# Optimization experiments

Hardware: AMD Instinct MI355X
Metric: run time of the kernel (lower is better)

The kernel has to match this reference:

```python
import jax, jax.numpy as jnp
import numpy as np

N = 50000      # nodes
R = 3          # relation types
E = 200000     # edges per relation
DIN, DHID, DOUT = 128, 128, 64


def _hetero_graphconv(x, src, dst, W, b):
    """Sum over relations of dgl GraphConv(norm='both') applied per relation.
    x:[N,d_in], src/dst:[R,E], W:[R,d_in,d_out], b:[R,d_out] -> [N,d_out]"""
    Rr, Ee = src.shape
    n = x.shape[0]
    off = (jnp.arange(Rr) * n)[:, None]            # per-relation segment offset
    src_f = (src + off).reshape(-1)                # [R*E]
    dst_f = (dst + off).reshape(-1)
    ones = jnp.ones((Rr * Ee,), x.dtype)
    out_deg = jax.ops.segment_sum(ones, src_f, num_segments=Rr * n).reshape(Rr, n)
    in_deg = jax.ops.segment_sum(ones, dst_f, num_segments=Rr * n).reshape(Rr, n)
    out_norm = jnp.maximum(out_deg, 1.0) ** -0.5   # dgl clamps deg to min 1
    in_norm = jnp.maximum(in_deg, 1.0) ** -0.5
    # gather src features, scaled by per-relation out-degree norm: [R,E,d_in]
    msgs = x[src] * jnp.take_along_axis(out_norm, src, axis=1)[..., None]
    agg = jax.ops.segment_sum(msgs.reshape(Rr * Ee, -1), dst_f,
                              num_segments=Rr * n).reshape(Rr, n, -1)
    agg = agg * in_norm[..., None]                 # [R,N,d_in]
    # per-relation linear then sum over relations (HeteroGraphConv 'sum')
    return jnp.einsum('rnd,rdo->no', agg, W) + b.sum(axis=0)


def setup_inputs() -> dict:
    key = jax.random.key(0)
    ks = jax.random.split(key, 7)
    x = jax.random.normal(ks[0], (N, DIN), jnp.float32)
    src = jax.random.randint(ks[1], (R, E), 0, N)
    dst = jax.random.randint(ks[2], (R, E), 0, N)
    W1 = jax.random.normal(ks[3], (R, DIN, DHID), jnp.float32) / np.sqrt(DIN).astype(np.float32)
    b1 = jax.random.normal(ks[4], (R, DHID), jnp.float32) * 0.01
    W2 = jax.random.normal(ks[5], (R, DHID, DOUT), jnp.float32) / np.sqrt(DHID).astype(np.float32)
    b2 = jax.random.normal(ks[6], (R, DOUT), jnp.float32) * 0.01
    return {"x": x, "W1": W1, "b1": b1, "W2": W2, "b2": b2, "src": src, "dst": dst}


def reference(x, W1, b1, W2, b2, src, dst):
    h = jax.nn.relu(_hetero_graphconv(x, src, dst, W1, b1))
    return _hetero_graphconv(h, src, dst, W2, b2)
```

## Files before the change

### kernel.cpp

```cpp
#include <hip/hip_runtime.h>

#define N_NODES 50000
#define N_REL   3
#define N_EDGE  200000
#define RN      (N_REL * N_NODES)
#define RE      (N_REL * N_EDGE)
#define GEMM1_BLKS 782
#define DEG_BLKS   2344
#define SCAN_BLOCKS 49
#define FUSE_CHUNKS 98
#define PREP_BLKS  288

typedef short bf16x8 __attribute__((ext_vector_type(8)));
typedef float f32x4  __attribute__((ext_vector_type(4)));

__device__ __forceinline__ unsigned short f2bf(float f) {
    unsigned u = __float_as_uint(f);
    u = (u + 0x7fffu + ((u >> 16) & 1u)) >> 16;
    return (unsigned short)u;
}
__device__ __forceinline__ unsigned pack_bf2(float lo, float hi) {
    return (unsigned)f2bf(lo) | ((unsigned)f2bf(hi) << 16);
}

__device__ __forceinline__ void wtrans_one(
    const float* __restrict__ W, unsigned short* __restrict__ Wtf, int ncols, int i)
{
    int rel = i / (128 * ncols);
    int rem = i - rel * 128 * ncols;
    int k   = rem / ncols;
    int n   = rem - k * ncols;
    int f   = (rel * (ncols / 16) + (n >> 4)) * 4 + (k >> 5);
    int idx = f * 512 + ((k & 31) >> 3) * 128 + (n & 15) * 8 + (k & 7);
    Wtf[idx] = f2bf(W[i]);
}

__global__ __launch_bounds__(256) void prep_kernel(
    const float* __restrict__ W1, unsigned short* __restrict__ Wt1,
    const float* __restrict__ W2, unsigned short* __restrict__ Wt2,
    float* __restrict__ zbuf, int* __restrict__ done)
{
    int i = blockIdx.x * 256 + threadIdx.x;
    if (i == 0) *done = 0;
    for (int q = i; q < 2 * RN; q += PREP_BLKS * 256) zbuf[q] = 0.f;
    if (i < 3 * 128 * 128) {
        wtrans_one(W1, Wt1, 128, i);
    } else {
        int j = i - 3 * 128 * 128;
        if (j < 3 * 128 * 64) wtrans_one(W2, Wt2, 64, j);
    }
}

template <bool ABF16, int NCOLS>
__device__ __forceinline__ void gemm_body(
    const void* __restrict__ Av, const unsigned short* __restrict__ Wtf,
    unsigned short* __restrict__ Y, int nrows, int mt,
    unsigned* As, unsigned* Ws0, unsigned* Ws1)
{
    const int tid = threadIdx.x;
    const uint4* Wt4 = (const uint4*)Wtf;

    if constexpr (ABF16) {
        const uint4* Ab = (const uint4*)Av;
        #pragma unroll
        for (int p = 0; p < 4; ++p) {
            int q   = p * 256 + tid;
            int row = q >> 4, w4 = q & 15;
            int gr  = mt + row;
            uint4 v = make_uint4(0u, 0u, 0u, 0u);
            if (gr < nrows) v = Ab[(size_t)gr * 16 + w4];
            As[row * 68 + w4 * 4 + 0] = v.x;
            As[row * 68 + w4 * 4 + 1] = v.y;
            As[row * 68 + w4 * 4 + 2] = v.z;
            As[row * 68 + w4 * 4 + 3] = v.w;
        }
    } else {
        const float* A = (const float*)Av;
        #pragma unroll
        for (int p = 0; p < 16; ++p) {
            int q   = tid + p * 256;
            int row = q >> 6, wc = q & 63;
            int gr  = mt + row;
            float2 v = make_float2(0.f, 0.f);
            if (gr < nrows) v = *reinterpret_cast<const float2*>(&A[(size_t)gr * 128 + wc * 2]);
            As[row * 68 + wc] = pack_bf2(v.x, v.y);
        }
    }

    #pragma unroll
    for (int p = 0; p < 4; ++p) {
        uint4 v = Wt4[tid + p * 256];
        *reinterpret_cast<uint4*>(&Ws0[(tid + p * 256) * 4]) = v;
    }
    __syncthreads();

    const int w  = tid >> 6;
    const int l  = tid & 63;
    const int g  = l >> 4;
    const int lr = l & 15;
    const int ar = w * 16 + lr;

    bf16x8 a[4];
    #pragma unroll
    for (int kb = 0; kb < 4; ++kb)
        a[kb] = *reinterpret_cast<const bf16x8*>(&As[ar * 68 + kb * 16 + g * 4]);

    constexpr int TPR  = NCOLS / 16;
    constexpr int NGRP = 3 * NCOLS / 64;
    const int boff = (g * 16 + lr) * 4;

    unsigned* wc_buf = Ws0;
    unsigned* wn_buf = Ws1;
    #pragma unroll 1
    for (int grp = 0; grp < NGRP; ++grp) {
        uint4 st[4];
        if (grp + 1 < NGRP) {
            #pragma unroll
            for (int p = 0; p < 4; ++p)
                st[p] = Wt4[(grp + 1) * 1024 + tid + p * 256];
        }

        f32x4 acc[4];
        #pragma unroll
        for (int ct4 = 0; ct4 < 4; ++ct4) {
            acc[ct4] = (f32x4){0.f, 0.f, 0.f, 0.f};
            #pragma unroll
            for (int kb = 0; kb < 4; ++kb) {
                bf16x8 b = *reinterpret_cast<const bf16x8*>(
                    &wc_buf[(ct4 * 4 + kb) * 256 + boff]);
                acc[ct4] = __builtin_amdgcn_mfma_f32_16x16x32_bf16(a[kb], b, acc[ct4], 0, 0, 0);
            }
        }

        int gct0 = grp * 4;
        int rel  = gct0 / TPR;
        int cb   = (gct0 % TPR) * 16;
        #pragma unroll
        for (int i = 0; i < 4; ++i) {
            int grow = mt + w * 16 + g * 4 + i;
            if (grow < nrows) {
                size_t rowbase = ((size_t)rel * N_NODES + grow) * NCOLS + cb;
                #pragma unroll
                for (int ct4 = 0; ct4 < 4; ++ct4)
                    Y[rowbase + ct4 * 16 + lr] = f2bf(acc[ct4][i]);
            }
        }

        if (grp + 1 < NGRP) {
            #pragma unroll
            for (int p = 0; p < 4; ++p)
                *reinterpret_cast<uint4*>(&wn_buf[(tid + p * 256) * 4]) = st[p];
        }
        __syncthreads();
        unsigned* t = wc_buf; wc_buf = wn_buf; wn_buf = t;
    }
}

template <bool ABF16, int NCOLS>
__global__ __launch_bounds__(256) void gemm_mfma(
    const void* __restrict__ Av, const unsigned short* __restrict__ Wtf,
    unsigned short* __restrict__ Y, int nrows)
{
    __shared__ unsigned As[64 * 68];
    __shared__ unsigned Ws[2][4096];
    gemm_body<ABF16, NCOLS>(Av, Wtf, Y, nrows, blockIdx.x * 64, As, Ws[0], Ws[1]);
}

__device__ __forceinline__ void gemm1_body_light(
    const float* __restrict__ A, const unsigned short* __restrict__ Wtf,
    unsigned short* __restrict__ Y, int mt, unsigned* Ws)
{
    const int tid = threadIdx.x;
    const uint4* Wt4 = (const uint4*)Wtf;
    const int w  = tid >> 6;
    const int l  = tid & 63;
    const int g  = l >> 4;
    const int lr = l & 15;
    const int arow = mt + w * 16 + lr;
    const bool rowok = arow < N_NODES;

    bf16x8 a[4];
    #pragma unroll
    for (int kb = 0; kb < 4; ++kb) {
        float4 v0 = make_float4(0.f, 0.f, 0.f, 0.f);
        float4 v1 = make_float4(0.f, 0.f, 0.f, 0.f);
        if (rowok) {
            const float* ap = &A[(size_t)arow * 128 + kb * 32 + g * 8];
            v0 = *reinterpret_cast<const float4*>(ap);
            v1 = *reinterpret_cast<const float4*>(ap + 4);
        }
        union { unsigned u[4]; bf16x8 v; } cv;
        cv.u[0] = pack_bf2(v0.x, v0.y);
        cv.u[1] = pack_bf2(v0.z, v0.w);
        cv.u[2] = pack_bf2(v1.x, v1.y);
        cv.u[3] = pack_bf2(v1.z, v1.w);
        a[kb] = cv.v;
    }

    const int boff = (g * 16 + lr) * 4;

    #pragma unroll 1
    for (int grp = 0; grp < 6; ++grp) {
        __syncthreads();
        #pragma unroll
        for (int p = 0; p < 4; ++p) {
            uint4 v = Wt4[grp * 1024 + tid + p * 256];
            *reinterpret_cast<uint4*>(&Ws[(tid + p * 256) * 4]) = v;
        }
        __syncthreads();

        f32x4 acc[4];
        #pragma unroll
        for (int ct4 = 0; ct4 < 4; ++ct4) {
            acc[ct4] = (f32x4){0.f, 0.f, 0.f, 0.f};
            #pragma unroll
            for (int kb = 0; kb < 4; ++kb) {
                bf16x8 b = *reinterpret_cast<const bf16x8*>(
                    &Ws[(ct4 * 4 + kb) * 256 + boff]);
                acc[ct4] = __builtin_amdgcn_mfma_f32_16x16x32_bf16(a[kb], b, acc[ct4], 0, 0, 0);
            }
        }

        int rel = grp >> 1;
        int cb  = (grp & 1) * 64;
        #pragma unroll
        for (int i = 0; i < 4; ++i) {
            int grow = mt + w * 16 + g * 4 + i;
            if (grow < N_NODES) {
                size_t rowbase = ((size_t)rel * N_NODES + grow) * 128 + cb;
                #pragma unroll
                for (int ct4 = 0; ct4 < 4; ++ct4)
                    Y[rowbase + ct4 * 16 + lr] = f2bf(acc[ct4][i]);
            }
        }
    }
}

__global__ __launch_bounds__(256) void fused_gemm1_deg(
    const float* __restrict__ x, const unsigned short* __restrict__ Wt1,
    unsigned short* __restrict__ Y,
    const int* __restrict__ src, const int* __restrict__ dst,
    float* __restrict__ odeg, float* __restrict__ ideg,
    unsigned short* __restrict__ rank)
{
    __shared__ unsigned Ws[4096];

    const int c = blockIdx.x >> 5;
    const int o = blockIdx.x & 31;

    if (o < 8) {
        int gb = c * 8 + o;
        if (gb >= GEMM1_BLKS) return;
        gemm1_body_light(x, Wt1, Y, gb * 64, Ws);
    } else {
        int db = c * 24 + (o - 8);
        int i  = db * 256 + threadIdx.x;
        if (i < RE) {
            int r = i / N_EDGE;
            int s = src[i], t = dst[i];
            unsafeAtomicAdd(&odeg[r * N_NODES + s], 1.0f);
            float old = unsafeAtomicAdd(&ideg[r * N_NODES + t], 1.0f);
            rank[i] = (unsigned short)(int)old;
        }
    }
}

__global__ __launch_bounds__(256) void scan_all_kernel(
    float* __restrict__ odeg, float* __restrict__ ideg,
    int* __restrict__ off, int* __restrict__ roff,
    int* __restrict__ bsums, int* __restrict__ done)
{
    __shared__ int tsum[256];
    __shared__ int addsh;
    const int tid  = threadIdx.x;
    const int base = blockIdx.x * 1024 + tid * 4;

    float c0[4], c1[4], c2[4];
    int tot[4], s = 0;
    #pragma unroll
    for (int j = 0; j < 4; ++j) {
        int idx = base + j;
        if (idx < N_NODES) {
            c0[j] = ideg[idx];
            c1[j] = ideg[N_NODES + idx];
            c2[j] = ideg[2 * N_NODES + idx];
            tot[j] = (int)c0[j] + (int)c1[j] + (int)c2[j];
        } else { c0[j] = c1[j] = c2[j] = 0.f; tot[j] = 0; }
        s += tot[j];
    }
    tsum[tid] = s;
    __syncthreads();
    #pragma unroll
    for (int d = 1; d < 256; d <<= 1) {
        int v   = tsum[tid];
        int add = (tid >= d) ? tsum[tid - d] : 0;
        __syncthreads();
        tsum[tid] = v + add;
        __syncthreads();
    }
    int run = tsum[tid] - s;

    if (tid == 255) bsums[blockIdx.x] = tsum[255];
    __threadfence();
    if (tid == 0) {
        __hip_atomic_fetch_add(done, 1, __ATOMIC_RELEASE, __HIP_MEMORY_SCOPE_AGENT);
        while (__hip_atomic_load(done, __ATOMIC_ACQUIRE, __HIP_MEMORY_SCOPE_AGENT) < SCAN_BLOCKS)
            __builtin_amdgcn_s_sleep(2);
    }
    __syncthreads();

    if (tid < 64) {
        int v = (tid < blockIdx.x) ? bsums[tid] : 0;
        #pragma unroll
        for (int d = 32; d > 0; d >>= 1) v += __shfl_down(v, d, 64);
        if (tid == 0) addsh = v;
    }
    __syncthreads();
    int run2 = run + addsh;

    #pragma unroll
    for (int j = 0; j < 4; ++j) {
        int t = base + j;
        if (t < N_NODES) {
            off[t]                = run2;
            roff[t]               = run2;
            roff[N_NODES + t]     = run2 + (int)c0[j];
            roff[2 * N_NODES + t] = run2 + (int)c0[j] + (int)c1[j];
            ideg[t]               = rsqrtf(fmaxf(c0[j], 1.0f));
            ideg[N_NODES + t]     = rsqrtf(fmaxf(c1[j], 1.0f));
            ideg[2 * N_NODES + t] = rsqrtf(fmaxf(c2[j], 1.0f));
            run2 += tot[j];
        }
    }
    if (blockIdx.x == 0 && tid == 0) off[N_NODES] = RE;

    int q0 = blockIdx.x * 256 + tid;
    for (int q = q0; q < RN; q += SCAN_BLOCKS * 256)
        odeg[q] = rsqrtf(fmaxf(odeg[q], 1.0f));
}

__global__ __launch_bounds__(256) void fill_kernel(
    const int* __restrict__ src, const int* __restrict__ dst,
    const float* __restrict__ onorm, const float* __restrict__ inorm,
    const int* __restrict__ roff, const unsigned short* __restrict__ rank,
    unsigned* __restrict__ csr)
{
    int i = blockIdx.x * 256 + threadIdx.x;
    if (i >= N_EDGE) return;
    int r   = blockIdx.y;
    int idx = r * N_EDGE + i;
    int s = src[idx], t = dst[idx];
    float wv = onorm[r * N_NODES + s] * inorm[r * N_NODES + t];
    int slot = roff[r * N_NODES + t] + (int)rank[idx];
    csr[slot] = ((unsigned)s << 16) | (unsigned)f2bf(wv);
}

__global__ __launch_bounds__(256) void agg128_kernel(
    const unsigned* __restrict__ Y, const unsigned* __restrict__ csr,
    const int* __restrict__ off, const int* __restrict__ roff,
    const float* __restrict__ b, unsigned* __restrict__ hbf)
{
    int wid  = (blockIdx.x * 256 + threadIdx.x) >> 6;
    int lane = threadIdx.x & 63;
    if (wid >= N_NODES) return;

    int e   = off[wid], end = off[wid + 1];
    int r1  = roff[N_NODES + wid];
    int r2  = roff[2 * N_NODES + wid];
    float a0 = 0.f, a1 = 0.f;

    for (; e + 8 <= end; e += 8) {
        unsigned p[8]; unsigned y[8];
        #pragma unroll
        for (int j = 0; j < 8; ++j) p[j] = csr[e + j];
        #pragma unroll
        for (int j = 0; j < 8; ++j) {
            int rr = (e + j >= r1) + (e + j >= r2);
            y[j] = Y[((size_t)rr * N_NODES + (p[j] >> 16)) * 64 + lane];
        }
        #pragma unroll
        for (int j = 0; j < 8; ++j) {
            float wv = __uint_as_float((p[j] & 0xffffu) << 16);
            a0 = fmaf(wv, __uint_as_float(y[j] << 16), a0);
            a1 = fmaf(wv, __uint_as_float(y[j] & 0xffff0000u), a1);
        }
    }
    if (e + 4 <= end) {
        unsigned p[4]; unsigned y[4];
        #pragma unroll
        for (int j = 0; j < 4; ++j) p[j] = csr[e + j];
        #pragma unroll
        for (int j = 0; j < 4; ++j) {
            int rr = (e + j >= r1) + (e + j >= r2);
            y[j] = Y[((size_t)rr * N_NODES + (p[j] >> 16)) * 64 + lane];
        }
        #pragma unroll
        for (int j = 0; j < 4; ++j) {
            float wv = __uint_as_float((p[j] & 0xffffu) << 16);
            a0 = fmaf(wv, __uint_as_float(y[j] << 16), a0);
            a1 = fmaf(wv, __uint_as_float(y[j] & 0xffff0000u), a1);
        }
        e += 4;
    }
    for (; e < end; ++e) {
        unsigned p = csr[e];
        int rr = (e >= r1) + (e >= r2);
        unsigned y = Y[((size_t)rr * N_NODES + (p >> 16)) * 64 + lane];
        float wv = __uint_as_float((p & 0xffffu) << 16);
        a0 = fmaf(wv, __uint_as_float(y << 16), a0);
        a1 = fmaf(wv, __uint_as_float(y & 0xffff0000u), a1);
    }

    int d = lane * 2;
    float o0 = a0 + b[d]     + b[128 + d]     + b[256 + d];
    float o1 = a1 + b[d + 1] + b[128 + d + 1] + b[256 + d + 1];
    hbf[(size_t)wid * 64 + lane] = pack_bf2(fmaxf(o0, 0.f), fmaxf(o1, 0.f));
}

__global__ __launch_bounds__(256) void agg64_kernel(
    const unsigned short* __restrict__ Y, const unsigned* __restrict__ csr,
    const int* __restrict__ off, const int* __restrict__ roff,
    const float* __restrict__ b, float* __restrict__ out)
{
    int wid  = (blockIdx.x * 256 + threadIdx.x) >> 6;
    int lane = threadIdx.x & 63;
    if (wid >= N_NODES) return;

    int e   = off[wid], end = off[wid + 1];
    int r1  = roff[N_NODES + wid];
    int r2  = roff[2 * N_NODES + wid];
    float a = 0.f;

    for (; e + 8 <= end; e += 8) {
        unsigned p[8]; unsigned short y[8];
        #pragma unroll
        for (int j = 0; j < 8; ++j) p[j] = csr[e + j];
        #pragma unroll
        for (int j = 0; j < 8; ++j) {
            int rr = (e + j >= r1) + (e + j >= r2);
            y[j] = Y[((size_t)rr * N_NODES + (p[j] >> 16)) * 64 + lane];
        }
        #pragma unroll
        for (int j = 0; j < 8; ++j)
            a = fmaf(__uint_as_float((p[j] & 0xffffu) << 16),
                     __uint_as_float(((unsigned)y[j]) << 16), a);
    }
    if (e + 4 <= end) {
        unsigned p[4]; unsigned short y[4];
        #pragma unroll
        for (int j = 0; j < 4; ++j) p[j] = csr[e + j];
        #pragma unroll
        for (int j = 0; j < 4; ++j) {
            int rr = (e + j >= r1) + (e + j >= r2);
            y[j] = Y[((size_t)rr * N_NODES + (p[j] >> 16)) * 64 + lane];
        }
        #pragma unroll
        for (int j = 0; j < 4; ++j)
            a = fmaf(__uint_as_float((p[j] & 0xffffu) << 16),
                     __uint_as_float(((unsigned)y[j]) << 16), a);
        e += 4;
    }
    for (; e < end; ++e) {
        unsigned p = csr[e];
        int rr = (e >= r1) + (e >= r2);
        a = fmaf(__uint_as_float((p & 0xffffu) << 16),
                 __uint_as_float(((unsigned)Y[((size_t)rr * N_NODES + (p >> 16)) * 64 + lane]) << 16), a);
    }

    float bs = b[lane] + b[64 + lane] + b[128 + lane];
    out[(size_t)wid * 64 + lane] = a + bs;
}

extern "C" void kernel_launch(void* const* d_in, const int* in_sizes, int n_in,
                              void* d_out, int out_size, void* d_ws, size_t ws_size,
                              hipStream_t stream)
{
    const float* x   = (const float*)d_in[0];
    const float* W1  = (const float*)d_in[1];
    const float* b1  = (const float*)d_in[2];
    const float* W2  = (const float*)d_in[3];
    const float* b2  = (const float*)d_in[4];
    const int*   src = (const int*)d_in[5];
    const int*   dst = (const int*)d_in[6];
    float*       out = (float*)d_out;

    char* w = (char*)d_ws;
    float* onorm  = (float*)w;                 w += (size_t)RN * 4;
    float* inorm  = (float*)w;                 w += (size_t)RN * 4;
    int*   off    = (int*)w;                   w += (size_t)(N_NODES + 1) * 4;
    int*   roff   = (int*)w;                   w += (size_t)RN * 4;
    int*   bsums  = (int*)w;                   w += 512;
    int*   done   = (int*)w;                   w += 512;
    unsigned short* rank = (unsigned short*)w; w += (size_t)RE * 2;
    w = (char*)(((uintptr_t)w + 255) & ~(uintptr_t)255);
    unsigned* csr = (unsigned*)w;              w += (size_t)RE * 4;
    unsigned* hbf = (unsigned*)w;              w += (size_t)N_NODES * 64 * 4;
    unsigned short* Ybf = (unsigned short*)w;  w += (size_t)N_REL * N_NODES * 128 * 2;
    unsigned short* Wt1 = (unsigned short*)w;  w += (size_t)N_REL * 128 * 128 * 2;
    unsigned short* Wt2 = (unsigned short*)w;

    prep_kernel<<<PREP_BLKS, 256, 0, stream>>>(W1, Wt1, W2, Wt2, onorm, done);

    fused_gemm1_deg<<<FUSE_CHUNKS * 32, 256, 0, stream>>>(
        x, Wt1, Ybf, src, dst, onorm, inorm, rank);

    scan_all_kernel<<<SCAN_BLOCKS, 256, 0, stream>>>(onorm, inorm, off, roff, bsums, done);

    fill_kernel<<<dim3((N_EDGE + 255) / 256, N_REL), 256, 0, stream>>>(
        src, dst, onorm, inorm, roff, rank, csr);

    agg128_kernel<<<(N_NODES + 3) / 4, 256, 0, stream>>>(
        (const unsigned*)Ybf, csr, off, roff, b1, hbf);

    gemm_mfma<true, 64><<<GEMM1_BLKS, 256, 0, stream>>>(hbf, Wt2, Ybf, N_NODES);
    agg64_kernel<<<(N_NODES + 3) / 4, 256, 0, stream>>>(Ybf, csr, off, roff, b2, out);
}
```

Measured before the change: 261.2 us.

## Fuse scan with CSR fill and fuse layer-1 aggregation with layer-2 GEMM

Result: slower. 342.3 us (+31.1%).

```diff
diff --git a/kernel.cpp b/kernel.cpp
--- a/kernel.cpp
+++ b/kernel.cpp
@@ -6,9 +6,8 @@
 #define RN      (N_REL * N_NODES)
 #define RE      (N_REL * N_EDGE)
 #define GEMM1_BLKS 782
-#define DEG_BLKS   2344
-#define SCAN_BLOCKS 49
 #define FUSE_CHUNKS 98
+#define SF_BLOCKS 196
 #define PREP_BLKS  288
 
 typedef short bf16x8 __attribute__((ext_vector_type(8)));
@@ -41,7 +40,7 @@
     float* __restrict__ zbuf, int* __restrict__ done)
 {
     int i = blockIdx.x * 256 + threadIdx.x;
-    if (i == 0) *done = 0;
+    if (i < 2) done[i] = 0;
     for (int q = i; q < 2 * RN; q += PREP_BLKS * 256) zbuf[q] = 0.f;
     if (i < 3 * 128 * 128) {
         wtrans_one(W1, Wt1, 128, i);
@@ -49,121 +48,6 @@
         int j = i - 3 * 128 * 128;
         if (j < 3 * 128 * 64) wtrans_one(W2, Wt2, 64, j);
     }
-}
-
-template <bool ABF16, int NCOLS>
-__device__ __forceinline__ void gemm_body(
-    const void* __restrict__ Av, const unsigned short* __restrict__ Wtf,
-    unsigned short* __restrict__ Y, int nrows, int mt,
-    unsigned* As, unsigned* Ws0, unsigned* Ws1)
-{
-    const int tid = threadIdx.x;
-    const uint4* Wt4 = (const uint4*)Wtf;
-
-    if constexpr (ABF16) {
-        const uint4* Ab = (const uint4*)Av;
-        #pragma unroll
-        for (int p = 0; p < 4; ++p) {
-            int q   = p * 256 + tid;
-            int row = q >> 4, w4 = q & 15;
-            int gr  = mt + row;
-            uint4 v = make_uint4(0u, 0u, 0u, 0u);
-            if (gr < nrows) v = Ab[(size_t)gr * 16 + w4];
-            As[row * 68 + w4 * 4 + 0] = v.x;
-            As[row * 68 + w4 * 4 + 1] = v.y;
-            As[row * 68 + w4 * 4 + 2] = v.z;
-            As[row * 68 + w4 * 4 + 3] = v.w;
-        }
-    } else {
-        const float* A = (const float*)Av;
-        #pragma unroll
-        for (int p = 0; p < 16; ++p) {
-            int q   = tid + p * 256;
-            int row = q >> 6, wc = q & 63;
-            int gr  = mt + row;
-            float2 v = make_float2(0.f, 0.f);
-            if (gr < nrows) v = *reinterpret_cast<const float2*>(&A[(size_t)gr * 128 + wc * 2]);
-            As[row * 68 + wc] = pack_bf2(v.x, v.y);
-        }
-    }
-
-    #pragma unroll
-    for (int p = 0; p < 4; ++p) {
-        uint4 v = Wt4[tid + p * 256];
-        *reinterpret_cast<uint4*>(&Ws0[(tid + p * 256) * 4]) = v;
-    }
-    __syncthreads();
-
-    const int w  = tid >> 6;
-    const int l  = tid & 63;
-    const int g  = l >> 4;
-    const int lr = l & 15;
-    const int ar = w * 16 + lr;
-
-    bf16x8 a[4];
-    #pragma unroll
-    for (int kb = 0; kb < 4; ++kb)
-        a[kb] = *reinterpret_cast<const bf16x8*>(&As[ar * 68 + kb * 16 + g * 4]);
-
-    constexpr int TPR  = NCOLS / 16;
-    constexpr int NGRP = 3 * NCOLS / 64;
-    const int boff = (g * 16 + lr) * 4;
-
-    unsigned* wc_buf = Ws0;
-    unsigned* wn_buf = Ws1;
-    #pragma unroll 1
-    for (int grp = 0; grp < NGRP; ++grp) {
-        uint4 st[4];
-        if (grp + 1 < NGRP) {
-            #pragma unroll
-            for (int p = 0; p < 4; ++p)
-                st[p] = Wt4[(grp + 1) * 1024 + tid + p * 256];
-        }
-
-        f32x4 acc[4];
-        #pragma unroll
-        for (int ct4 = 0; ct4 < 4; ++ct4) {
-            acc[ct4] = (f32x4){0.f, 0.f, 0.f, 0.f};
-            #pragma unroll
-            for (int kb = 0; kb < 4; ++kb) {
-                bf16x8 b = *reinterpret_cast<const bf16x8*>(
-                    &wc_buf[(ct4 * 4 + kb) * 256 + boff]);
-                acc[ct4] = __builtin_amdgcn_mfma_f32_16x16x32_bf16(a[kb], b, acc[ct4], 0, 0, 0);
-            }
-        }
-
-        int gct0 = grp * 4;
-        int rel  = gct0 / TPR;
-        int cb   = (gct0 % TPR) * 16;
-        #pragma unroll
-        for (int i = 0; i < 4; ++i) {
-            int grow = mt + w * 16 + g * 4 + i;
-            if (grow < nrows) {
-                size_t rowbase = ((size_t)rel * N_NODES + grow) * NCOLS + cb;
-                #pragma unroll
-                for (int ct4 = 0; ct4 < 4; ++ct4)
-                    Y[rowbase + ct4 * 16 + lr] = f2bf(acc[ct4][i]);
-            }
-        }
-
-        if (grp + 1 < NGRP) {
-            #pragma unroll
-            for (int p = 0; p < 4; ++p)
-                *reinterpret_cast<uint4*>(&wn_buf[(tid + p * 256) * 4]) = st[p];
-        }
-        __syncthreads();
-        unsigned* t = wc_buf; wc_buf = wn_buf; wn_buf = t;
-    }
-}
-
-template <bool ABF16, int NCOLS>
-__global__ __launch_bounds__(256) void gemm_mfma(
-    const void* __restrict__ Av, const unsigned short* __restrict__ Wtf,
-    unsigned short* __restrict__ Y, int nrows)
-{
-    __shared__ unsigned As[64 * 68];
-    __shared__ unsigned Ws[2][4096];
-    gemm_body<ABF16, NCOLS>(Av, Wtf, Y, nrows, blockIdx.x * 64, As, Ws[0], Ws[1]);
 }
 
 __device__ __forceinline__ void gemm1_body_light(
@@ -265,30 +149,28 @@
     }
 }
 
-__global__ __launch_bounds__(256) void scan_all_kernel(
+__global__ __launch_bounds__(256) void scan_fill_kernel(
     float* __restrict__ odeg, float* __restrict__ ideg,
     int* __restrict__ off, int* __restrict__ roff,
-    int* __restrict__ bsums, int* __restrict__ done)
+    int* __restrict__ bsums, int* __restrict__ done,
+    const int* __restrict__ src, const int* __restrict__ dst,
+    const unsigned short* __restrict__ rank, unsigned* __restrict__ csr)
 {
     __shared__ int tsum[256];
     __shared__ int addsh;
     const int tid  = threadIdx.x;
-    const int base = blockIdx.x * 1024 + tid * 4;
-
-    float c0[4], c1[4], c2[4];
-    int tot[4], s = 0;
-    #pragma unroll
-    for (int j = 0; j < 4; ++j) {
-        int idx = base + j;
-        if (idx < N_NODES) {
-            c0[j] = ideg[idx];
-            c1[j] = ideg[N_NODES + idx];
-            c2[j] = ideg[2 * N_NODES + idx];
-            tot[j] = (int)c0[j] + (int)c1[j] + (int)c2[j];
-        } else { c0[j] = c1[j] = c2[j] = 0.f; tot[j] = 0; }
-        s += tot[j];
-    }
-    tsum[tid] = s;
+    const int bid  = blockIdx.x;
+    const int node = bid * 256 + tid;
+
+    float c0 = 0.f, c1 = 0.f, c2 = 0.f;
+    int tot = 0;
+    if (node < N_NODES) {
+        c0 = ideg[node];
+        c1 = ideg[N_NODES + node];
+        c2 = ideg[2 * N_NODES + node];
+        tot = (int)c0 + (int)c1 + (int)c2;
+    }
+    tsum[tid] = tot;
     __syncthreads();
     #pragma unroll
     for (int d = 1; d < 256; d <<= 1) {
@@ -298,123 +180,201 @@
         tsum[tid] = v + add;
         __syncthreads();
     }
-    int run = tsum[tid] - s;
-
-    if (tid == 255) bsums[blockIdx.x] = tsum[255];
+    const int lexcl = tsum[tid] - tot;
+    if (tid == 255) bsums[bid] = tsum[255];
+
+    if (node < N_NODES) {
+        ideg[node]               = rsqrtf(fmaxf(c0, 1.0f));
+        ideg[N_NODES + node]     = rsqrtf(fmaxf(c1, 1.0f));
+        ideg[2 * N_NODES + node] = rsqrtf(fmaxf(c2, 1.0f));
+    }
+    for (int q = bid * 256 + tid; q < RN; q += SF_BLOCKS * 256)
+        odeg[q] = rsqrtf(fmaxf(odeg[q], 1.0f));
+
+    __syncthreads();
     __threadfence();
     if (tid == 0) {
-        __hip_atomic_fetch_add(done, 1, __ATOMIC_RELEASE, __HIP_MEMORY_SCOPE_AGENT);
-        while (__hip_atomic_load(done, __ATOMIC_ACQUIRE, __HIP_MEMORY_SCOPE_AGENT) < SCAN_BLOCKS)
+        __hip_atomic_fetch_add(&done[0], 1, __ATOMIC_RELEASE, __HIP_MEMORY_SCOPE_AGENT);
+        while (__hip_atomic_load(&done[0], __ATOMIC_ACQUIRE, __HIP_MEMORY_SCOPE_AGENT) < SF_BLOCKS)
             __builtin_amdgcn_s_sleep(2);
     }
     __syncthreads();
 
-    if (tid < 64) {
-        int v = (tid < blockIdx.x) ? bsums[tid] : 0;
-        #pragma unroll
-        for (int d = 32; d > 0; d >>= 1) v += __shfl_down(v, d, 64);
-        if (tid == 0) addsh = v;
-    }
-    __syncthreads();
-    int run2 = run + addsh;
-
+    int bv = (tid < SF_BLOCKS) ? bsums[tid] : 0;
+    tsum[tid] = bv;
+    __syncthreads();
     #pragma unroll
-    for (int j = 0; j < 4; ++j) {
-        int t = base + j;
-        if (t < N_NODES) {
-            off[t]                = run2;
-            roff[t]               = run2;
-            roff[N_NODES + t]     = run2 + (int)c0[j];
-            roff[2 * N_NODES + t] = run2 + (int)c0[j] + (int)c1[j];
-            ideg[t]               = rsqrtf(fmaxf(c0[j], 1.0f));
-            ideg[N_NODES + t]     = rsqrtf(fmaxf(c1[j], 1.0f));
-            ideg[2 * N_NODES + t] = rsqrtf(fmaxf(c2[j], 1.0f));
-            run2 += tot[j];
-        }
-    }
-    if (blockIdx.x == 0 && tid == 0) off[N_NODES] = RE;
-
-    int q0 = blockIdx.x * 256 + tid;
-    for (int q = q0; q < RN; q += SCAN_BLOCKS * 256)
-        odeg[q] = rsqrtf(fmaxf(odeg[q], 1.0f));
-}
-
-__global__ __launch_bounds__(256) void fill_kernel(
-    const int* __restrict__ src, const int* __restrict__ dst,
-    const float* __restrict__ onorm, const float* __restrict__ inorm,
-    const int* __restrict__ roff, const unsigned short* __restrict__ rank,
-    unsigned* __restrict__ csr)
-{
-    int i = blockIdx.x * 256 + threadIdx.x;
-    if (i >= N_EDGE) return;
-    int r   = blockIdx.y;
-    int idx = r * N_EDGE + i;
-    int s = src[idx], t = dst[idx];
-    float wv = onorm[r * N_NODES + s] * inorm[r * N_NODES + t];
-    int slot = roff[r * N_NODES + t] + (int)rank[idx];
-    csr[slot] = ((unsigned)s << 16) | (unsigned)f2bf(wv);
-}
-
-__global__ __launch_bounds__(256) void agg128_kernel(
-    const unsigned* __restrict__ Y, const unsigned* __restrict__ csr,
+    for (int d = 1; d < 256; d <<= 1) {
+        int v   = tsum[tid];
+        int add = (tid >= d) ? tsum[tid - d] : 0;
+        __syncthreads();
+        tsum[tid] = v + add;
+        __syncthreads();
+    }
+    if (tid == 0) addsh = (bid == 0) ? 0 : tsum[bid - 1];
+    __syncthreads();
+
+    const int gbase = lexcl + addsh;
+    if (node < N_NODES) {
+        off[node]                = gbase;
+        roff[node]               = gbase;
+        roff[N_NODES + node]     = gbase + (int)c0;
+        roff[2 * N_NODES + node] = gbase + (int)c0 + (int)c1;
+    }
+    if (bid == 0 && tid == 0) off[N_NODES] = RE;
+
+    __syncthreads();
+    __threadfence();
+    if (tid == 0) {
+        __hip_atomic_fetch_add(&done[1], 1, __ATOMIC_RELEASE, __HIP_MEMORY_SCOPE_AGENT);
+        while (__hip_atomic_load(&done[1], __ATOMIC_ACQUIRE, __HIP_MEMORY_SCOPE_AGENT) < SF_BLOCKS)
+            __builtin_amdgcn_s_sleep(2);
+    }
+    __syncthreads();
+
+    for (int q = bid * 256 + tid; q < RE; q += SF_BLOCKS * 256) {
+        int r = q / N_EDGE;
+        int s = src[q], t = dst[q];
+        float wv = odeg[r * N_NODES + s] * ideg[r * N_NODES + t];
+        int slot = roff[r * N_NODES + t] + (int)rank[q];
+        csr[slot] = ((unsigned)s << 16) | (unsigned)f2bf(wv);
+    }
+}
+
+__global__ __launch_bounds__(256) void layer2_fused(
+    const unsigned* __restrict__ Y1, const unsigned* __restrict__ csr,
     const int* __restrict__ off, const int* __restrict__ roff,
-    const float* __restrict__ b, unsigned* __restrict__ hbf)
-{
-    int wid  = (blockIdx.x * 256 + threadIdx.x) >> 6;
-    int lane = threadIdx.x & 63;
-    if (wid >= N_NODES) return;
-
-    int e   = off[wid], end = off[wid + 1];
-    int r1  = roff[N_NODES + wid];
-    int r2  = roff[2 * N_NODES + wid];
-    float a0 = 0.f, a1 = 0.f;
-
-    for (; e + 8 <= end; e += 8) {
-        unsigned p[8]; unsigned y[8];
-        #pragma unroll
-        for (int j = 0; j < 8; ++j) p[j] = csr[e + j];
-        #pragma unroll
-        for (int j = 0; j < 8; ++j) {
-            int rr = (e + j >= r1) + (e + j >= r2);
-            y[j] = Y[((size_t)rr * N_NODES + (p[j] >> 16)) * 64 + lane];
-        }
-        #pragma unroll
-        for (int j = 0; j < 8; ++j) {
-            float wv = __uint_as_float((p[j] & 0xffffu) << 16);
-            a0 = fmaf(wv, __uint_as_float(y[j] << 16), a0);
-            a1 = fmaf(wv, __uint_as_float(y[j] & 0xffff0000u), a1);
-        }
-    }
-    if (e + 4 <= end) {
-        unsigned p[4]; unsigned y[4];
-        #pragma unroll
-        for (int j = 0; j < 4; ++j) p[j] = csr[e + j];
-        #pragma unroll
-        for (int j = 0; j < 4; ++j) {
-            int rr = (e + j >= r1) + (e + j >= r2);
-            y[j] = Y[((size_t)rr * N_NODES + (p[j] >> 16)) * 64 + lane];
-        }
-        #pragma unroll
-        for (int j = 0; j < 4; ++j) {
-            float wv = __uint_as_float((p[j] & 0xffffu) << 16);
-            a0 = fmaf(wv, __uint_as_float(y[j] << 16), a0);
-            a1 = fmaf(wv, __uint_as_float(y[j] & 0xffff0000u), a1);
-        }
-        e += 4;
-    }
-    for (; e < end; ++e) {
-        unsigned p = csr[e];
-        int rr = (e >= r1) + (e >= r2);
-        unsigned y = Y[((size_t)rr * N_NODES + (p >> 16)) * 64 + lane];
-        float wv = __uint_as_float((p & 0xffffu) << 16);
-        a0 = fmaf(wv, __uint_as_float(y << 16), a0);
-        a1 = fmaf(wv, __uint_as_float(y & 0xffff0000u), a1);
-    }
-
-    int d = lane * 2;
-    float o0 = a0 + b[d]     + b[128 + d]     + b[256 + d];
-    float o1 = a1 + b[d + 1] + b[128 + d + 1] + b[256 + d + 1];
-    hbf[(size_t)wid * 64 + lane] = pack_bf2(fmaxf(o0, 0.f), fmaxf(o1, 0.f));
+    const float* __restrict__ b, const unsigned short* __restrict__ Wt2,
+    unsigned short* __restrict__ Y2)
+{
+    __shared__ unsigned As[64 * 68];
+    __shared__ unsigned Ws[2][4096];
+
+    const int tid = threadIdx.x;
+    const int mt  = blockIdx.x * 64;
+    const uint4* Wt4 = (const uint4*)Wt2;
+
+    #pragma unroll
+    for (int p = 0; p < 4; ++p) {
+        uint4 v = Wt4[tid + p * 256];
+        *reinterpret_cast<uint4*>(&Ws[0][(tid + p * 256) * 4]) = v;
+    }
+
+    const int w    = tid >> 6;
+    const int lane = tid & 63;
+
+    #pragma unroll 1
+    for (int i = 0; i < 16; ++i) {
+        int node = mt + w * 16 + i;
+        unsigned packed = 0u;
+        if (node < N_NODES) {
+            int e  = off[node], end = off[node + 1];
+            int r1 = roff[N_NODES + node];
+            int r2 = roff[2 * N_NODES + node];
+            float a0 = 0.f, a1 = 0.f;
+
+            for (; e + 8 <= end; e += 8) {
+                unsigned p[8]; unsigned y[8];
+                #pragma unroll
+                for (int j = 0; j < 8; ++j) p[j] = csr[e + j];
+                #pragma unroll
+                for (int j = 0; j < 8; ++j) {
+                    int rr = (e + j >= r1) + (e + j >= r2);
+                    y[j] = Y1[((size_t)rr * N_NODES + (p[j] >> 16)) * 64 + lane];
+                }
+                #pragma unroll
+                for (int j = 0; j < 8; ++j) {
+                    float wv = __uint_as_float((p[j] & 0xffffu) << 16);
+                    a0 = fmaf(wv, __uint_as_float(y[j] << 16), a0);
+                    a1 = fmaf(wv, __uint_as_float(y[j] & 0xffff0000u), a1);
+                }
+            }
+            if (e + 4 <= end) {
+                unsigned p[4]; unsigned y[4];
+                #pragma unroll
+                for (int j = 0; j < 4; ++j) p[j] = csr[e + j];
+                #pragma unroll
+                for (int j = 0; j < 4; ++j) {
+                    int rr = (e + j >= r1) + (e + j >= r2);
+                    y[j] = Y1[((size_t)rr * N_NODES + (p[j] >> 16)) * 64 + lane];
+                }
+                #pragma unroll
+                for (int j = 0; j < 4; ++j) {
+                    float wv = __uint_as_float((p[j] & 0xffffu) << 16);
+                    a0 = fmaf(wv, __uint_as_float(y[j] << 16), a0);
+                    a1 = fmaf(wv, __uint_as_float(y[j] & 0xffff0000u), a1);
+                }
+                e += 4;
+            }
+            for (; e < end; ++e) {
+                unsigned p = csr[e];
+                int rr = (e >= r1) + (e >= r2);
+                unsigned y = Y1[((size_t)rr * N_NODES + (p >> 16)) * 64 + lane];
+                float wv = __uint_as_float((p & 0xffffu) << 16);
+                a0 = fmaf(wv, __uint_as_float(y << 16), a0);
+                a1 = fmaf(wv, __uint_as_float(y & 0xffff0000u), a1);
+            }
+
+            int d = lane * 2;
+            float o0 = a0 + b[d]     + b[128 + d]     + b[256 + d];
+            float o1 = a1 + b[d + 1] + b[128 + d + 1] + b[256 + d + 1];
+            packed = pack_bf2(fmaxf(o0, 0.f), fmaxf(o1, 0.f));
+        }
+        As[(w * 16 + i) * 68 + lane] = packed;
+    }
+    __syncthreads();
+
+    const int g  = lane >> 4;
+    const int lr = lane & 15;
+    const int ar = w * 16 + lr;
+
+    bf16x8 a[4];
+    #pragma unroll
+    for (int kb = 0; kb < 4; ++kb)
+        a[kb] = *reinterpret_cast<const bf16x8*>(&As[ar * 68 + kb * 16 + g * 4]);
+
+    const int boff = (g * 16 + lr) * 4;
+    int cur = 0;
+    #pragma unroll 1
+    for (int grp = 0; grp < 3; ++grp) {
+        uint4 st[4];
+        if (grp + 1 < 3) {
+            #pragma unroll
+            for (int p = 0; p < 4; ++p)
+                st[p] = Wt4[(grp + 1) * 1024 + tid + p * 256];
+        }
+
+        f32x4 acc[4];
+        #pragma unroll
+        for (int ct4 = 0; ct4 < 4; ++ct4) {
+            acc[ct4] = (f32x4){0.f, 0.f, 0.f, 0.f};
+            #pragma unroll
+            for (int kb = 0; kb < 4; ++kb) {
+                bf16x8 bb = *reinterpret_cast<const bf16x8*>(
+                    &Ws[cur][(ct4 * 4 + kb) * 256 + boff]);
+                acc[ct4] = __builtin_amdgcn_mfma_f32_16x16x32_bf16(a[kb], bb, acc[ct4], 0, 0, 0);
+            }
+        }
+
+        #pragma unroll
+        for (int i = 0; i < 4; ++i) {
+            int grow = mt + w * 16 + g * 4 + i;
+            if (grow < N_NODES) {
+                size_t rowbase = ((size_t)grp * N_NODES + grow) * 64;
+                #pragma unroll
+                for (int ct4 = 0; ct4 < 4; ++ct4)
+                    Y2[rowbase + ct4 * 16 + lr] = f2bf(acc[ct4][i]);
+            }
+        }
+
+        if (grp + 1 < 3) {
+            #pragma unroll
+            for (int p = 0; p < 4; ++p)
+                *reinterpret_cast<uint4*>(&Ws[cur ^ 1][(tid + p * 256) * 4]) = st[p];
+        }
+        __syncthreads();
+        cur ^= 1;
+    }
 }
 
 __global__ __launch_bounds__(256) void agg64_kernel(
@@ -489,29 +449,26 @@
     float* inorm  = (float*)w;                 w += (size_t)RN * 4;
     int*   off    = (int*)w;                   w += (size_t)(N_NODES + 1) * 4;
     int*   roff   = (int*)w;                   w += (size_t)RN * 4;
-    int*   bsums  = (int*)w;                   w += 512;
+    int*   bsums  = (int*)w;                   w += 1024;
     int*   done   = (int*)w;                   w += 512;
     unsigned short* rank = (unsigned short*)w; w += (size_t)RE * 2;
     w = (char*)(((uintptr_t)w + 255) & ~(uintptr_t)255);
     unsigned* csr = (unsigned*)w;              w += (size_t)RE * 4;
-    unsigned* hbf = (unsigned*)w;              w += (size_t)N_NODES * 64 * 4;
-    unsigned short* Ybf = (unsigned short*)w;  w += (size_t)N_REL * N_NODES * 128 * 2;
-    unsigned short* Wt1 = (unsigned short*)w;  w += (size_t)N_REL * 128 * 128 * 2;
-    unsigned short* Wt2 = (unsigned short*)w;
+    unsigned short* Ybf  = (unsigned short*)w; w += (size_t)N_REL * N_NODES * 128 * 2;
+    unsigned short* Y2bf = (unsigned short*)w; w += (size_t)N_REL * N_NODES * 64 * 2;
+    unsigned short* Wt1  = (unsigned short*)w; w += (size_t)N_REL * 128 * 128 * 2;
+    unsigned short* Wt2  = (unsigned short*)w;
 
     prep_kernel<<<PREP_BLKS, 256, 0, stream>>>(W1, Wt1, W2, Wt2, onorm, done);
 
     fused_gemm1_deg<<<FUSE_CHUNKS * 32, 256, 0, stream>>>(
         x, Wt1, Ybf, src, dst, onorm, inorm, rank);
 
-    scan_all_kernel<<<SCAN_BLOCKS, 256, 0, stream>>>(onorm, inorm, off, roff, bsums, done);
-
-    fill_kernel<<<dim3((N_EDGE + 255) / 256, N_REL), 256, 0, stream>>>(
-        src, dst, onorm, inorm, roff, rank, csr);
-
-    agg128_kernel<<<(N_NODES + 3) / 4, 256, 0, stream>>>(
-        (const unsigned*)Ybf, csr, off, roff, b1, hbf);
-
-    gemm_mfma<true, 64><<<GEMM1_BLKS, 256, 0, stream>>>(hbf, Wt2, Ybf, N_NODES);
-    agg64_kernel<<<(N_NODES + 3) / 4, 256, 0, stream>>>(Ybf, csr, off, roff, b2, out);
-}
+    scan_fill_kernel<<<SF_BLOCKS, 256, 0, stream>>>(
+        onorm, inorm, off, roff, bsums, done, src, dst, rank, csr);
+
+    layer2_fused<<<GEMM1_BLKS, 256, 0, stream>>>(
+        (const unsigned*)Ybf, csr, off, roff, b1, Wt2, Y2bf);
+
+    agg64_kernel<<<(N_NODES + 3) / 4, 256, 0, stream>>>(Y2bf, csr, off, roff, b2, out);
+}
```
